# Performance work log

Measured on AMD Instinct MI355X. Metric: run time of the kernel, lower is better.

## Reference

```python
import jax, jax.numpy as jnp
import numpy as np

D_MODEL = 1024
N_HEADS = 16
D_K = D_MODEL // N_HEADS  # 64
ROPE_BASE = 10000.0
MASK_FILL = -1e9


def _rope_cos_sin(seq_len, d_k, dtype):
    # inv_freq over even dims, freqs = outer(t, inv_freq): [S, d_k//2]
    inv_freq = 1.0 / (ROPE_BASE ** (jnp.arange(0, d_k, 2, dtype=jnp.float32) / d_k))
    freqs = jnp.arange(seq_len, dtype=jnp.float32)[:, None] * inv_freq[None, :]
    # broadcast to full d_k (rotate_half convention: same freq for x1 and x2 halves)
    cos = jnp.concatenate([jnp.cos(freqs), jnp.cos(freqs)], axis=-1).astype(dtype)
    sin = jnp.concatenate([jnp.sin(freqs), jnp.sin(freqs)], axis=-1).astype(dtype)
    return cos, sin  # each [S, d_k]


def _apply_rope(x, cos, sin):
    # x: [B, H, S, d_k]; rotate_half: (x1, x2) -> (-x2, x1)
    x1, x2 = jnp.split(x, 2, axis=-1)
    rot = jnp.concatenate([-x2, x1], axis=-1)
    return x * cos[None, None] + rot * sin[None, None]


def setup_inputs() -> dict:
    key = jax.random.key(0)
    kx, kqkv, ko = jax.random.split(key, 3)
    x = jax.random.normal(kx, (1, 4096, D_MODEL), dtype=jnp.float32)
    # nn.Linear weight shape [out, in]; y = x @ W.T
    s = 1.0 / np.sqrt(D_MODEL)
    W_qkv = jax.random.uniform(kqkv, (3 * D_MODEL, D_MODEL), jnp.float32, -s, s)
    W_o = jax.random.uniform(ko, (D_MODEL, D_MODEL), jnp.float32, -s, s)
    return {"x": x, "W_qkv": W_qkv, "W_o": W_o}


def reference(x, W_qkv, W_o):
    B, S, _ = x.shape
    qkv = jnp.einsum("bsd,ed->bse", x, W_qkv)  # [B, S, 3*d_model]
    Q, K, V = jnp.split(qkv, 3, axis=-1)
    # [B, S, H, d_k] -> [B, H, S, d_k]
    reshape = lambda t: t.reshape(B, S, N_HEADS, D_K).transpose(0, 2, 1, 3)
    Q, K, V = reshape(Q), reshape(K), reshape(V)
    cos, sin = _rope_cos_sin(S, D_K, x.dtype)
    Q = _apply_rope(Q, cos, sin)
    K = _apply_rope(K, cos, sin)
    scores = jnp.einsum("bhqd,bhkd->bhqk", Q, K) / jnp.sqrt(jnp.asarray(D_K, x.dtype))
    causal = jnp.tril(jnp.ones((S, S), dtype=bool))
    scores = jnp.where(causal[None, None], scores, jnp.asarray(MASK_FILL, x.dtype))
    attn = jax.nn.softmax(scores, axis=-1)  # dropout inactive at inference
    out = jnp.einsum("bhqk,bhkd->bhqd", attn, V)
    out = out.transpose(0, 2, 1, 3).reshape(B, S, D_MODEL)
    return jnp.einsum("bsd,ed->bse", out, W_o)
```

## Files before the change

### kernel.cpp

```cpp
#include <hip/hip_runtime.h>


typedef __attribute__((ext_vector_type(8)))  short  short8;
typedef __attribute__((ext_vector_type(4)))  float  f32x4;
typedef __attribute__((ext_vector_type(16))) float  f32x16;
typedef __attribute__((ext_vector_type(4)))  float  float4v;
typedef __attribute__((ext_vector_type(4)))  unsigned short ushort4v;
typedef __attribute__((ext_vector_type(4)))  unsigned int   uint4v;

#define S_LEN 4096
#define DMODEL 1024
#define NHEADS 16
#define DKH 64

#define QSCALE 0.18033688011112042f

__device__ __forceinline__ unsigned short f2bf(float f) {
  unsigned u = __builtin_bit_cast(unsigned, f);
  u += 0x7FFFu + ((u >> 16) & 1u);
  return (unsigned short)(u >> 16);
}
__device__ __forceinline__ float bf2f(unsigned short h) {
  return __builtin_bit_cast(float, ((unsigned)h) << 16);
}

#define GLDS16(gsrc, ldst)                                                   \
  __builtin_amdgcn_global_load_lds(                                          \
      (const __attribute__((address_space(1))) void*)(gsrc),                 \
      (__attribute__((address_space(3))) void*)(ldst), 16, 0, 0)

__global__ void cvt_bf16_kernel(const float* __restrict__ src,
                                unsigned short* __restrict__ dst, int n4) {
  int i = blockIdx.x * blockDim.x + threadIdx.x;
  if (i >= n4) return;
  float4v v = reinterpret_cast<const float4v*>(src)[i];
  ushort4v o;
  o[0] = f2bf(v[0]); o[1] = f2bf(v[1]); o[2] = f2bf(v[2]); o[3] = f2bf(v[3]);
  reinterpret_cast<ushort4v*>(dst)[i] = o;
}

template<bool OUT_BF16>
__global__ __launch_bounds__(256) void gemm_lds(const unsigned short* __restrict__ A,
                                                const unsigned short* __restrict__ B,
                                                void* __restrict__ Cp,
                                                int M, int N, int K) {
  __shared__ __align__(16) unsigned short As[128 * 32];
  __shared__ __align__(16) unsigned short Bs[128 * 32];

  const int tid = threadIdx.x;
  const int l = tid & 63, w = tid >> 6;
  const int wr = w >> 1, wc = w & 1;
  const int bm = blockIdx.y * 128, bn = blockIdx.x * 128;
  const int lr = l & 15, lk = (l >> 4) * 8;

  f32x4 acc[4][4] = {};

  const unsigned short* Ag0 = A + (size_t)(bm + (tid >> 2)) * K + (tid & 3) * 8;
  const unsigned short* Ag1 = A + (size_t)(bm + 64 + (tid >> 2)) * K + (tid & 3) * 8;
  const unsigned short* Bg0 = B + (size_t)(bn + (tid >> 2)) * K + (tid & 3) * 8;
  const unsigned short* Bg1 = B + (size_t)(bn + 64 + (tid >> 2)) * K + (tid & 3) * 8;
  unsigned short* Ad0 = As + tid * 8;
  unsigned short* Ad1 = As + (tid + 256) * 8;
  unsigned short* Bd0 = Bs + tid * 8;
  unsigned short* Bd1 = Bs + (tid + 256) * 8;

  const unsigned short* Afr = As + (wr * 64 + lr) * 32 + lk;
  const unsigned short* Bfr = Bs + (wc * 64 + lr) * 32 + lk;

  for (int k0 = 0; k0 < K; k0 += 32) {
    GLDS16(Ag0 + k0, Ad0);
    GLDS16(Ag1 + k0, Ad1);
    GLDS16(Bg0 + k0, Bd0);
    GLDS16(Bg1 + k0, Bd1);
    __syncthreads();

    short8 af[4], bfr[4];
#pragma unroll
    for (int mi = 0; mi < 4; mi++) af[mi]  = *(const short8*)(Afr + mi * 16 * 32);
#pragma unroll
    for (int ni = 0; ni < 4; ni++) bfr[ni] = *(const short8*)(Bfr + ni * 16 * 32);

#pragma unroll
    for (int mi = 0; mi < 4; mi++)
#pragma unroll
      for (int ni = 0; ni < 4; ni++)
        acc[mi][ni] = __builtin_amdgcn_mfma_f32_16x16x32_bf16(af[mi], bfr[ni],
                                                              acc[mi][ni], 0, 0, 0);
    __syncthreads();
  }

  const int row0 = bm + wr * 64 + (l >> 4) * 4;
  const int col0 = bn + wc * 64 + lr;
#pragma unroll
  for (int mi = 0; mi < 4; mi++)
#pragma unroll
    for (int ni = 0; ni < 4; ni++)
#pragma unroll
      for (int j = 0; j < 4; j++) {
        size_t idx = (size_t)(row0 + mi * 16 + j) * N + (col0 + ni * 16);
        if (OUT_BF16) ((unsigned short*)Cp)[idx] = f2bf(acc[mi][ni][j]);
        else          ((float*)Cp)[idx]          = acc[mi][ni][j];
      }
}

__global__ void rope_split_kernel(const unsigned short* __restrict__ qkv,
                                  unsigned short* __restrict__ Qr,
                                  unsigned short* __restrict__ Kr,
                                  unsigned short* __restrict__ Vt) {
  int gid = blockIdx.x * blockDim.x + threadIdx.x;
  int s = gid >> 10;
  int e = gid & 1023;
  int h = e >> 6, d = e & 63;
  size_t base = (size_t)s * 3072;

  float q = bf2f(qkv[base + e]);
  float k = bf2f(qkv[base + 1024 + e]);

  int i = d & 31;
  float inv = expf(-(float)(2 * i) * (9.2103403719761836f / 64.0f));
  float ang = (float)s * inv;
  float sn, cs;
  sincosf(ang, &sn, &cs);

  int ep = (d < 32) ? (e + 32) : (e - 32);
  float qp = bf2f(qkv[base + ep]);
  float kp = bf2f(qkv[base + 1024 + ep]);

  float qo, ko;
  if (d < 32) { qo = q * cs - qp * sn; ko = k * cs - kp * sn; }
  else        { qo = q * cs + qp * sn; ko = k * cs + kp * sn; }

  size_t oidx = ((size_t)h * S_LEN + s) * DKH + d;
  Qr[oidx] = f2bf(qo * QSCALE);
  Kr[oidx] = f2bf(ko);
  Vt[((size_t)h * DKH + d) * S_LEN + s] = qkv[base + 2048 + e];
}

__global__ __launch_bounds__(256) void flash_attn_kernel(const unsigned short* __restrict__ Qr,
                                                         const unsigned short* __restrict__ Kr,
                                                         const unsigned short* __restrict__ Vt,
                                                         unsigned short* __restrict__ O) {
  __shared__ __align__(16) char smem[32768];

  const int tid = threadIdx.x;
  const int l  = tid & 63;
  const int w  = tid >> 6;
  const int r  = l & 31;
  const int hi = l >> 5;

  const int bx    = blockIdx.x;
  const int xcd   = bx & 7;
  const int j     = bx >> 3;
  const int h     = xcd * 2 + (j & 1);
  const int qtile = 127 - (j >> 1);
  const int q0    = qtile * 32;

  const unsigned short* Qh = Qr + (size_t)h * S_LEN * DKH;
  const unsigned short* Kh = Kr + (size_t)h * S_LEN * DKH;
  const unsigned short* Vh = Vt + (size_t)h * DKH * S_LEN;

  const int krow  = tid >> 3;
  const int kcE   = (((tid & 7) * 16) ^ ((krow & 7) << 4)) >> 1;
  const size_t kbase = (size_t)krow * DKH + kcE;
  const int vrow  = tid >> 4;
  const int vcE   = (((tid & 15) * 16) ^ ((vrow & 7) << 4)) >> 1;
  const size_t vbase = (size_t)vrow * S_LEN + vcE;

  const int sw      = (r & 7) << 4;
  const int kfbyte  = (w * 32 + r) * 128;
  const int vfbyte0 = r * 256;
  const int vfbyte1 = (r + 32) * 256;
  const int vcol    = w * 64 + hi * 16;

  short8 qf[4];
  {
    const unsigned short* qb = Qh + (size_t)(q0 + r) * 64 + hi * 8;
#pragma unroll
    for (int dc = 0; dc < 4; dc++) qf[dc] = *(const short8*)(qb + dc * 16);
  }

  f32x16 acc0 = {}, acc1 = {};
  float m = -1e30f, lsum = 0.0f;

  const int nwin = (qtile >> 2) + 1;
  for (int it = 0; it < nwin; it++) {
    {
      const unsigned short* Kg = Kh + (size_t)it * 128 * DKH;
      const unsigned short* Vg = Vh + it * 128;
#pragma unroll
      for (int i = 0; i < 4; i++) {
        GLDS16(Kg + kbase + (size_t)i * 32 * DKH, smem + i * 4096 + tid * 16);
        GLDS16(Vg + vbase + (size_t)i * 16 * S_LEN,
               smem + 16384 + i * 4096 + tid * 16);
      }
    }
    __syncthreads();

    const int c = 4 * it + w;
    if (c <= qtile) {
      short8 kf[4], vf[4];
#pragma unroll
      for (int dc = 0; dc < 4; dc++)
        kf[dc] = *(const short8*)(smem + kfbyte + ((dc * 32 + hi * 16) ^ sw));
#pragma unroll
      for (int kc = 0; kc < 2; kc++) {
        vf[kc]     = *(const short8*)(smem + 16384 + vfbyte0 + ((vcol + kc * 32) ^ sw));
        vf[2 + kc] = *(const short8*)(smem + 16384 + vfbyte1 + ((vcol + kc * 32) ^ sw));
      }

      f32x16 st = {};
      __builtin_amdgcn_s_setprio(1);
      st = __builtin_amdgcn_mfma_f32_32x32x16_bf16(kf[0], qf[0], st, 0, 0, 0);
      st = __builtin_amdgcn_mfma_f32_32x32x16_bf16(kf[1], qf[1], st, 0, 0, 0);
      st = __builtin_amdgcn_mfma_f32_32x32x16_bf16(kf[2], qf[2], st, 0, 0, 0);
      st = __builtin_amdgcn_mfma_f32_32x32x16_bf16(kf[3], qf[3], st, 0, 0, 0);
      __builtin_amdgcn_s_setprio(0);

      if (c == qtile) {
#pragma unroll
        for (int reg = 0; reg < 16; reg++) {
          const int koff = (reg & 3) + 8 * (reg >> 2) + 4 * hi;
          if (koff > r) st[reg] = -1e30f;
        }
      }

      float t0 = fmaxf(fmaxf(st[0],  st[1]),  st[2]);
      float t1 = fmaxf(fmaxf(st[3],  st[4]),  st[5]);
      float t2 = fmaxf(fmaxf(st[6],  st[7]),  st[8]);
      float t3 = fmaxf(fmaxf(st[9],  st[10]), st[11]);
      float t4 = fmaxf(fmaxf(st[12], st[13]), st[14]);
      float pm = fmaxf(fmaxf(fmaxf(t0, t1), fmaxf(t2, t3)), fmaxf(t4, st[15]));
      pm = fmaxf(pm, __shfl_xor(pm, 32));

      if (!__all(pm <= m + 8.0f)) {
        float mn  = fmaxf(m, pm);
        float scl = exp2f(m - mn);
        m = mn;
        lsum *= scl;
#pragma unroll
        for (int reg = 0; reg < 16; reg++) { acc0[reg] *= scl; acc1[reg] *= scl; }
      }

      float p[16];
#pragma unroll
      for (int reg = 0; reg < 16; reg++) p[reg] = exp2f(st[reg] - m);

      float s2[8];
#pragma unroll
      for (int i = 0; i < 8; i++) s2[i] = p[2 * i] + p[2 * i + 1];
#pragma unroll
      for (int i = 0; i < 4; i++) s2[i] = s2[i] + s2[i + 4];
      float rs = (s2[0] + s2[2]) + (s2[1] + s2[3]);
      rs += __shfl_xor(rs, 32);
      lsum += rs;

      unsigned wd[8];
#pragma unroll
      for (int i = 0; i < 8; i++) {
        asm("v_cvt_pk_bf16_f32 %0, %1, %2" : "=v"(wd[i]) : "v"(p[2 * i]), "v"(p[2 * i + 1]));
      }
      unsigned pw[8];
#pragma unroll
      for (int i = 0; i < 8; i++) pw[i] = __shfl_xor(wd[i], 32);

      uint4v u0, u1;
      u0[0] = hi ? pw[2] : wd[0];
      u0[1] = hi ? pw[3] : wd[1];
      u0[2] = hi ? wd[2] : pw[0];
      u0[3] = hi ? wd[3] : pw[1];
      u1[0] = hi ? pw[6] : wd[4];
      u1[1] = hi ? pw[7] : wd[5];
      u1[2] = hi ? wd[6] : pw[4];
      u1[3] = hi ? wd[7] : pw[5];
      short8 pa0 = __builtin_bit_cast(short8, u0);
      short8 pa1 = __builtin_bit_cast(short8, u1);

      __builtin_amdgcn_s_setprio(1);
      acc0 = __builtin_amdgcn_mfma_f32_32x32x16_bf16(vf[0], pa0, acc0, 0, 0, 0);
      acc0 = __builtin_amdgcn_mfma_f32_32x32x16_bf16(vf[1], pa1, acc0, 0, 0, 0);
      acc1 = __builtin_amdgcn_mfma_f32_32x32x16_bf16(vf[2], pa0, acc1, 0, 0, 0);
      acc1 = __builtin_amdgcn_mfma_f32_32x32x16_bf16(vf[3], pa1, acc1, 0, 0, 0);
      __builtin_amdgcn_s_setprio(0);
    }
    __syncthreads();
  }

  unsigned (*oaccp)[32][33] = (unsigned (*)[32][33])smem;
  float* mlm = (float*)(smem + 16896);
  float* mll = (float*)(smem + 17408);

  if (hi == 0) { mlm[w * 32 + r] = m; mll[w * 32 + r] = lsum; }
#pragma unroll
  for (int i = 0; i < 8; i++) {
    const int widx = 4 * (i >> 1) + 2 * hi + (i & 1);
    unsigned ua, ub;
    asm("v_cvt_pk_bf16_f32 %0, %1, %2" : "=v"(ua) : "v"(acc0[2 * i]), "v"(acc0[2 * i + 1]));
    asm("v_cvt_pk_bf16_f32 %0, %1, %2" : "=v"(ub) : "v"(acc1[2 * i]), "v"(acc1[2 * i + 1]));
    oaccp[w][r][widx]      = ua;
    oaccp[w][r][16 + widx] = ub;
  }
  __syncthreads();

  const int q  = tid >> 3;
  const int c0 = (tid & 7) * 4;
  const float m0 = mlm[q], m1 = mlm[32 + q], m2 = mlm[64 + q], m3 = mlm[96 + q];
  const float mmax = fmaxf(fmaxf(m0, m1), fmaxf(m2, m3));
  const float sc[4] = {exp2f(m0 - mmax), exp2f(m1 - mmax),
                       exp2f(m2 - mmax), exp2f(m3 - mmax)};
  const float ltot = sc[0] * mll[q] + sc[1] * mll[32 + q] +
                     sc[2] * mll[64 + q] + sc[3] * mll[96 + q];
  const float rinv = 1.0f / ltot;

  float vs[8] = {};
#pragma unroll
  for (int wv = 0; wv < 4; wv++) {
#pragma unroll
    for (int i = 0; i < 4; i++) {
      unsigned u = oaccp[wv][q][c0 + i];
      vs[2 * i]     += sc[wv] * __builtin_bit_cast(float, u << 16);
      vs[2 * i + 1] += sc[wv] * __builtin_bit_cast(float, u & 0xFFFF0000u);
    }
  }
  short8 ov;
#pragma unroll
  for (int i = 0; i < 8; i++) ov[i] = (short)f2bf(vs[i] * rinv);
  *(short8*)(O + (size_t)(q0 + q) * DMODEL + h * 64 + c0 * 2) = ov;
}

extern "C" void kernel_launch(void* const* d_in, const int* in_sizes, int n_in,
                              void* d_out, int out_size, void* d_ws, size_t ws_size,
                              hipStream_t stream) {
  (void)in_sizes; (void)n_in; (void)out_size; (void)ws_size;
  const float* x    = (const float*)d_in[0];
  const float* Wqkv = (const float*)d_in[1];
  const float* Wo   = (const float*)d_in[2];
  float* out = (float*)d_out;

  char* ws = (char*)d_ws;
  const size_t MB = 1u << 20;
  unsigned short* x_bf    = (unsigned short*)(ws + 0 * MB);
  unsigned short* wqkv_bf = (unsigned short*)(ws + 8 * MB);
  unsigned short* wo_bf   = (unsigned short*)(ws + 14 * MB);
  unsigned short* qkv_bf  = (unsigned short*)(ws + 16 * MB);
  unsigned short* Qr      = (unsigned short*)(ws + 40 * MB);
  unsigned short* Kr      = (unsigned short*)(ws + 48 * MB);
  unsigned short* Vt      = (unsigned short*)(ws + 56 * MB);
  unsigned short* Obf     = (unsigned short*)(ws + 64 * MB);

  const int n_x = 4096 * 1024, n_wqkv = 3072 * 1024, n_wo = 1024 * 1024;
  cvt_bf16_kernel<<<(n_x / 4 + 255) / 256, 256, 0, stream>>>(x, x_bf, n_x / 4);
  cvt_bf16_kernel<<<(n_wqkv / 4 + 255) / 256, 256, 0, stream>>>(Wqkv, wqkv_bf, n_wqkv / 4);
  cvt_bf16_kernel<<<(n_wo / 4 + 255) / 256, 256, 0, stream>>>(Wo, wo_bf, n_wo / 4);

  gemm_lds<true><<<dim3(3072 / 128, 4096 / 128), 256, 0, stream>>>(x_bf, wqkv_bf, qkv_bf,
                                                                   4096, 3072, 1024);
  rope_split_kernel<<<(4096 * 1024) / 256, 256, 0, stream>>>(qkv_bf, Qr, Kr, Vt);

  flash_attn_kernel<<<2048, 256, 0, stream>>>(Qr, Kr, Vt, Obf);

  gemm_lds<false><<<dim3(1024 / 128, 4096 / 128), 256, 0, stream>>>(Obf, wo_bf, out,
                                                                    4096, 1024, 1024);
}
```

Measured before the change: 194.3 us.

## Double-buffer flash-attention K/V loads, merge conversions, pair RoPE halves

Flash attention now uses two LDS buffers and prefetches the next K/V window while the current one is computed, which removes one barrier per iteration and hides global-load latency. The three fp32-to-bf16 conversion launches are merged into one kernel. The RoPE kernel now has each thread handle both rotate-half partners, halving the thread count and cutting redundant loads. Doubling LDS to 64KB per block may reduce occupancy.

After: 207.7 us. 1.07x slower.

```diff
diff --git a/kernel.cpp b/kernel.cpp
--- a/kernel.cpp
+++ b/kernel.cpp
@@ -29,14 +29,18 @@
       (const __attribute__((address_space(1))) void*)(gsrc),                 \
       (__attribute__((address_space(3))) void*)(ldst), 16, 0, 0)
 
-__global__ void cvt_bf16_kernel(const float* __restrict__ src,
-                                unsigned short* __restrict__ dst, int n4) {
+__global__ void cvt_bf16_all(const float* __restrict__ x,    unsigned short* __restrict__ xb,
+                             const float* __restrict__ wq,   unsigned short* __restrict__ wqb,
+                             const float* __restrict__ wo,   unsigned short* __restrict__ wob) {
   int i = blockIdx.x * blockDim.x + threadIdx.x;
-  if (i >= n4) return;
-  float4v v = reinterpret_cast<const float4v*>(src)[i];
+  const float* src; unsigned short* dst; int off;
+  if (i < 1048576)               { src = x;  dst = xb;  off = i; }
+  else if (i < 1048576 + 786432) { src = wq; dst = wqb; off = i - 1048576; }
+  else                           { src = wo; dst = wob; off = i - 1048576 - 786432; }
+  float4v v = reinterpret_cast<const float4v*>(src)[off];
   ushort4v o;
   o[0] = f2bf(v[0]); o[1] = f2bf(v[1]); o[2] = f2bf(v[2]); o[3] = f2bf(v[3]);
-  reinterpret_cast<ushort4v*>(dst)[i] = o;
+  reinterpret_cast<ushort4v*>(dst)[off] = o;
 }
 
 template<bool OUT_BF16>
@@ -108,39 +112,39 @@
                                   unsigned short* __restrict__ Kr,
                                   unsigned short* __restrict__ Vt) {
   int gid = blockIdx.x * blockDim.x + threadIdx.x;
-  int s = gid >> 10;
-  int e = gid & 1023;
-  int h = e >> 6, d = e & 63;
+  int s = gid >> 9;
+  int t = gid & 511;
+  int h = t >> 5, d = t & 31;
+  int e = h * 64 + d;
   size_t base = (size_t)s * 3072;
 
-  float q = bf2f(qkv[base + e]);
-  float k = bf2f(qkv[base + 1024 + e]);
-
-  int i = d & 31;
-  float inv = expf(-(float)(2 * i) * (9.2103403719761836f / 64.0f));
+  float q1 = bf2f(qkv[base + e]);
+  float q2 = bf2f(qkv[base + e + 32]);
+  float k1 = bf2f(qkv[base + 1024 + e]);
+  float k2 = bf2f(qkv[base + 1024 + e + 32]);
+
+  float inv = expf(-(float)(2 * d) * (9.2103403719761836f / 64.0f));
   float ang = (float)s * inv;
   float sn, cs;
   sincosf(ang, &sn, &cs);
 
-  int ep = (d < 32) ? (e + 32) : (e - 32);
-  float qp = bf2f(qkv[base + ep]);
-  float kp = bf2f(qkv[base + 1024 + ep]);
-
-  float qo, ko;
-  if (d < 32) { qo = q * cs - qp * sn; ko = k * cs - kp * sn; }
-  else        { qo = q * cs + qp * sn; ko = k * cs + kp * sn; }
-
-  size_t oidx = ((size_t)h * S_LEN + s) * DKH + d;
-  Qr[oidx] = f2bf(qo * QSCALE);
-  Kr[oidx] = f2bf(ko);
-  Vt[((size_t)h * DKH + d) * S_LEN + s] = qkv[base + 2048 + e];
+  float qo1 = q1 * cs - q2 * sn, qo2 = q2 * cs + q1 * sn;
+  float ko1 = k1 * cs - k2 * sn, ko2 = k2 * cs + k1 * sn;
+
+  size_t o1 = ((size_t)h * S_LEN + s) * DKH + d;
+  Qr[o1]      = f2bf(qo1 * QSCALE);
+  Qr[o1 + 32] = f2bf(qo2 * QSCALE);
+  Kr[o1]      = f2bf(ko1);
+  Kr[o1 + 32] = f2bf(ko2);
+  Vt[((size_t)h * DKH + d) * S_LEN + s]        = qkv[base + 2048 + e];
+  Vt[((size_t)h * DKH + d + 32) * S_LEN + s]   = qkv[base + 2048 + e + 32];
 }
 
 __global__ __launch_bounds__(256) void flash_attn_kernel(const unsigned short* __restrict__ Qr,
                                                          const unsigned short* __restrict__ Kr,
                                                          const unsigned short* __restrict__ Vt,
                                                          unsigned short* __restrict__ O) {
-  __shared__ __align__(16) char smem[32768];
+  __shared__ __align__(16) char smem[2][32768];
 
   const int tid = threadIdx.x;
   const int l  = tid & 63;
@@ -161,10 +165,11 @@
 
   const int krow  = tid >> 3;
   const int kcE   = (((tid & 7) * 16) ^ ((krow & 7) << 4)) >> 1;
-  const size_t kbase = (size_t)krow * DKH + kcE;
   const int vrow  = tid >> 4;
   const int vcE   = (((tid & 15) * 16) ^ ((vrow & 7) << 4)) >> 1;
-  const size_t vbase = (size_t)vrow * S_LEN + vcE;
+
+  const unsigned short* kg = Kh + (size_t)krow * DKH + kcE;
+  const unsigned short* vg = Vh + (size_t)vrow * S_LEN + vcE;
 
   const int sw      = (r & 7) << 4;
   const int kfbyte  = (w * 32 + r) * 128;
@@ -183,29 +188,40 @@
   float m = -1e30f, lsum = 0.0f;
 
   const int nwin = (qtile >> 2) + 1;
+
+#pragma unroll
+  for (int i = 0; i < 4; i++) {
+    GLDS16(kg + (size_t)i * 32 * DKH,  smem[0] + i * 4096 + tid * 16);
+    GLDS16(vg + (size_t)i * 16 * S_LEN, smem[0] + 16384 + i * 4096 + tid * 16);
+  }
+  kg += 128 * DKH;
+  vg += 128;
+  __syncthreads();
+
+  int buf = 0;
   for (int it = 0; it < nwin; it++) {
-    {
-      const unsigned short* Kg = Kh + (size_t)it * 128 * DKH;
-      const unsigned short* Vg = Vh + it * 128;
+    if (it + 1 < nwin) {
+      char* sd = smem[buf ^ 1];
 #pragma unroll
       for (int i = 0; i < 4; i++) {
-        GLDS16(Kg + kbase + (size_t)i * 32 * DKH, smem + i * 4096 + tid * 16);
-        GLDS16(Vg + vbase + (size_t)i * 16 * S_LEN,
-               smem + 16384 + i * 4096 + tid * 16);
-      }
+        GLDS16(kg + (size_t)i * 32 * DKH,  sd + i * 4096 + tid * 16);
+        GLDS16(vg + (size_t)i * 16 * S_LEN, sd + 16384 + i * 4096 + tid * 16);
+      }
+      kg += 128 * DKH;
+      vg += 128;
     }
-    __syncthreads();
-
+
+    const char* sm = smem[buf];
     const int c = 4 * it + w;
     if (c <= qtile) {
       short8 kf[4], vf[4];
 #pragma unroll
       for (int dc = 0; dc < 4; dc++)
-        kf[dc] = *(const short8*)(smem + kfbyte + ((dc * 32 + hi * 16) ^ sw));
+        kf[dc] = *(const short8*)(sm + kfbyte + ((dc * 32 + hi * 16) ^ sw));
 #pragma unroll
       for (int kc = 0; kc < 2; kc++) {
-        vf[kc]     = *(const short8*)(smem + 16384 + vfbyte0 + ((vcol + kc * 32) ^ sw));
-        vf[2 + kc] = *(const short8*)(smem + 16384 + vfbyte1 + ((vcol + kc * 32) ^ sw));
+        vf[kc]     = *(const short8*)(sm + 16384 + vfbyte0 + ((vcol + kc * 32) ^ sw));
+        vf[2 + kc] = *(const short8*)(sm + 16384 + vfbyte1 + ((vcol + kc * 32) ^ sw));
       }
 
       f32x16 st = {};
@@ -282,12 +298,14 @@
       acc1 = __builtin_amdgcn_mfma_f32_32x32x16_bf16(vf[3], pa1, acc1, 0, 0, 0);
       __builtin_amdgcn_s_setprio(0);
     }
+
     __syncthreads();
-  }
-
-  unsigned (*oaccp)[32][33] = (unsigned (*)[32][33])smem;
-  float* mlm = (float*)(smem + 16896);
-  float* mll = (float*)(smem + 17408);
+    buf ^= 1;
+  }
+
+  unsigned (*oaccp)[32][33] = (unsigned (*)[32][33])smem[0];
+  float* mlm = (float*)(smem[0] + 16896);
+  float* mll = (float*)(smem[0] + 17408);
 
   if (hi == 0) { mlm[w * 32 + r] = m; mll[w * 32 + r] = lsum; }
 #pragma unroll
@@ -347,14 +365,11 @@
   unsigned short* Vt      = (unsigned short*)(ws + 56 * MB);
   unsigned short* Obf     = (unsigned short*)(ws + 64 * MB);
 
-  const int n_x = 4096 * 1024, n_wqkv = 3072 * 1024, n_wo = 1024 * 1024;
-  cvt_bf16_kernel<<<(n_x / 4 + 255) / 256, 256, 0, stream>>>(x, x_bf, n_x / 4);
-  cvt_bf16_kernel<<<(n_wqkv / 4 + 255) / 256, 256, 0, stream>>>(Wqkv, wqkv_bf, n_wqkv / 4);
-  cvt_bf16_kernel<<<(n_wo / 4 + 255) / 256, 256, 0, stream>>>(Wo, wo_bf, n_wo / 4);
+  cvt_bf16_all<<<8192, 256, 0, stream>>>(x, x_bf, Wqkv, wqkv_bf, Wo, wo_bf);
 
   gemm_lds<true><<<dim3(3072 / 128, 4096 / 128), 256, 0, stream>>>(x_bf, wqkv_bf, qkv_bf,
                                                                    4096, 3072, 1024);
-  rope_split_kernel<<<(4096 * 1024) / 256, 256, 0, stream>>>(qkv_bf, Qr, Kr, Vt);
+  rope_split_kernel<<<8192, 256, 0, stream>>>(qkv_bf, Qr, Kr, Vt);
 
   flash_attn_kernel<<<2048, 256, 0, stream>>>(Qr, Kr, Vt, Obf);
 
```
